# Optimization experiments

Measured on AMD Instinct MI355X. Metric: run time of the kernel, lower is better.

Reference implementation:

```python
import jax, jax.numpy as jnp
import numpy as np

H, W, C_IN, C_ADD = 721, 1440, 78, 8
N_NODES, K = 5882, 128
DAY_OF_YEAR = 182.5  # module default time_of_year
LN_EPS = 1e-5        # haiku LayerNorm default
NORM_EPS = 1e-7


def setup_inputs() -> dict:
    key = jax.random.key(0)
    ks = jax.random.split(key, 4)
    return {
        "var_grid": jax.random.normal(ks[0], (H, W, C_IN), dtype=jnp.float32),
        "nearby_idx": jax.random.randint(ks[1], (N_NODES, K), 0, H * W),
        "input_means": jnp.zeros((C_IN + C_ADD,), jnp.float32),
        "input_stds": jnp.ones((C_IN + C_ADD,), jnp.float32),
        "W1": jax.random.normal(ks[2], (C_IN + C_ADD, 256), dtype=jnp.float32) * 0.1,
        "b1": jnp.zeros((256,), jnp.float32),
        "ln_scale": jnp.ones((256,), jnp.float32),
        "ln_offset": jnp.zeros((256,), jnp.float32),
        "W2": jax.random.normal(ks[3], (256, 256), dtype=jnp.float32) * 0.1,
        "b2": jnp.zeros((256,), jnp.float32),
    }


def _additional_features(h, w):
    # 8 extra channels: sin/cos of lat/lon, normalized day-of-year, 3 zero pads
    lat = jnp.linspace(-90.0, 90.0, h)
    lon = jnp.linspace(0.0, 360.0, w)
    lat2d = jnp.broadcast_to(lat[:, None], (h, w))
    lon2d = jnp.broadcast_to(lon[None, :], (h, w))
    lat_r, lon_r = jnp.radians(lat2d), jnp.radians(lon2d)
    day = jnp.float32(DAY_OF_YEAR / 365.0)
    z = jnp.zeros((h, w), jnp.float32)
    return jnp.stack([
        jnp.sin(lat_r), jnp.cos(lat_r), jnp.sin(lon_r), jnp.cos(lon_r),
        jnp.full((h, w), day, jnp.float32), z, z, z,
    ], axis=-1)  # [H, W, 8]


def reference(var_grid, nearby_idx, input_means, input_stds,
              W1, b1, ln_scale, ln_offset, W2, b2):
    h, w, c = var_grid.shape
    add = _additional_features(h, w)                       # [H, W, 8]
    flat = jnp.concatenate([var_grid, add], -1).reshape(h * w, c + C_ADD)
    gathered = flat[nearby_idx]                            # [N, K, 86] irregular gather
    x = (gathered - input_means) / (input_stds + NORM_EPS)
    hidden = jax.nn.relu(jnp.einsum('nkc,cd->nkd', x, W1) + b1)
    mu = hidden.mean(-1, keepdims=True)
    var = hidden.var(-1, keepdims=True)
    hidden = (hidden - mu) * jax.lax.rsqrt(var + LN_EPS) * ln_scale + ln_offset
    nodes = jnp.einsum('nkd,de->nke', hidden, W2) + b2     # [N, K, 256]
    return nodes
```

## Files before the change

### kernel.cpp

```cpp
#include <hip/hip_runtime.h>
#include <hip/hip_bf16.h>
#include <math.h>

#define GH 721
#define GW 1440
#define C_IN 78
#define NNODES 5882
#define KNEIGH 128
#define M_TOTAL (NNODES * KNEIGH)
#define TM 128
#define NBLOCKS (M_TOTAL / TM)

typedef __attribute__((ext_vector_type(8))) short bf16x8;
typedef __attribute__((ext_vector_type(4))) float f32x4;

__device__ __forceinline__ unsigned short f2bf(float x) {
    __hip_bfloat16 b = __float2bfloat16(x);
    union { __hip_bfloat16 h; unsigned short u; } cv; cv.h = b; return cv.u;
}

__global__ void prep_kernel(const float* __restrict__ W1, const float* __restrict__ W2,
                            const float* __restrict__ means, const float* __restrict__ stds,
                            const float* __restrict__ b1,
                            unsigned short* __restrict__ bp1, unsigned short* __restrict__ bp2,
                            float* __restrict__ latT, float* __restrict__ lonT,
                            float* __restrict__ b1p)
{
    const int NB1 = 3 * 4 * 256 * 8;
    const int NB2 = 8 * 4 * 256 * 8;
    const int NTOT = NB1 + NB2 + GH + GW + 256;
    for (int e = blockIdx.x * blockDim.x + threadIdx.x; e < NTOT;
         e += gridDim.x * blockDim.x) {
        if (e < NB1) {
            int j = e & 7, c = (e >> 3) & 255, o = (e >> 11) & 3, s = e >> 13;
            int k = s * 32 + o * 8 + j;
            float v = 0.f;
            if (k < 82) v = W1[k * 256 + c] / (stds[k] + 1e-7f);
            bp1[e] = f2bf(v);
        } else if (e < NB1 + NB2) {
            int t = e - NB1;
            int j = t & 7, c = (t >> 3) & 255, o = (t >> 11) & 3, s = t >> 13;
            int k = s * 32 + o * 8 + j;
            bp2[t] = f2bf(W2[k * 256 + c]);
        } else if (e < NB1 + NB2 + GH) {
            int h = e - NB1 - NB2;
            float r = (-90.f + 0.25f * (float)h) * 0.017453292519943295f;
            latT[2 * h]     = sinf(r);
            latT[2 * h + 1] = cosf(r);
        } else if (e < NB1 + NB2 + GH + GW) {
            int w = e - NB1 - NB2 - GH;
            float r = ((float)w * (360.f / 1439.f)) * 0.017453292519943295f;
            lonT[2 * w]     = sinf(r);
            lonT[2 * w + 1] = cosf(r);
        } else {
            int c = e - NB1 - NB2 - GH - GW;
            float acc = b1[c];
            #pragma unroll 1
            for (int k = 0; k < 86; ++k) {
                float inv = 1.f / (stds[k] + 1e-7f);
                float w = W1[k * 256 + c] * inv;
                acc -= means[k] * w;
                if (k == 82) acc += 0.5f * w;
            }
            b1p[c] = acc;
        }
    }
}

__global__ __launch_bounds__(512, 4)
void fused_kernel(const float* __restrict__ var_grid, const int* __restrict__ idxs,
                  const unsigned short* __restrict__ bp1, const unsigned short* __restrict__ bp2,
                  const float* __restrict__ latT, const float* __restrict__ lonT,
                  const float* __restrict__ b1p, const float* __restrict__ lnS,
                  const float* __restrict__ lnO, const float* __restrict__ b2,
                  float* __restrict__ out)
{
    __shared__ __align__(16) char smem[TM * 256 * 2];
    __shared__ float red[2][4][TM];
    unsigned short* h_lds = (unsigned short*)smem;
    unsigned short (*x_lds)[104] = (unsigned short (*)[104])smem;
    float* otile = (float*)smem;

    const int tid  = threadIdx.x;
    const int lane = tid & 63;
    const int wave = tid >> 6;
    const int wr   = wave >> 2;
    const int wc   = wave & 3;
    const int l15  = lane & 15;
    const int lg   = lane >> 4;
    const int wbase = wc * 64;
    const int rbase = wr * 64;
    const long block0 = (long)blockIdx.x * TM;

    {
        const int row = tid >> 2, p = tid & 3;
        const int idx = idxs[block0 + row];
        const int hh = idx / GW;
        const int ww = idx - hh * GW;
        const float* src = var_grid + (long)idx * C_IN;
        float2 g[10];
        #pragma unroll
        for (int t = 0; t < 10; ++t) {
            const int q = p + 4 * t;
            if (q < 39) g[t] = *(const float2*)(src + 2 * q);
        }
        float2 tail;
        tail.x = latT[2 * hh]; tail.y = latT[2 * hh + 1];
        float2 tail2; tail2.x = lonT[2 * ww]; tail2.y = lonT[2 * ww + 1];
        unsigned int* xrow = (unsigned int*)&x_lds[row][0];
        #pragma unroll
        for (int t = 0; t < 12; ++t) {
            const int q = p + 4 * t;
            float v0, v1;
            if (q < 39)      { v0 = g[t].x; v1 = g[t].y; }
            else if (q == 39){ v0 = tail.x;  v1 = tail.y; }
            else if (q == 40){ v0 = tail2.x; v1 = tail2.y; }
            else             { v0 = 0.f; v1 = 0.f; }
            xrow[q] = ((unsigned int)f2bf(v1) << 16) | (unsigned int)f2bf(v0);
        }
    }

    float b1v[4], lsv[4], lov[4], b2v[4];
    #pragma unroll
    for (int nf = 0; nf < 4; ++nf) {
        int col = wbase + nf * 16 + l15;
        b1v[nf] = b1p[col]; lsv[nf] = lnS[col]; lov[nf] = lnO[col]; b2v[nf] = b2[col];
    }
    __syncthreads();

    f32x4 acc[4][4];
    #pragma unroll
    for (int mf = 0; mf < 4; ++mf)
        #pragma unroll
        for (int nf = 0; nf < 4; ++nf) acc[mf][nf] = (f32x4){0.f, 0.f, 0.f, 0.f};

    bf16x8 bw[4], bwn[4];
    #pragma unroll
    for (int nf = 0; nf < 4; ++nf)
        bw[nf] = *(const bf16x8*)(bp1 + ((size_t)(lg * 256) + wbase + nf * 16 + l15) * 8);

    #pragma unroll
    for (int s = 0; s < 3; ++s) {
        if (s < 2)
            #pragma unroll
            for (int nf = 0; nf < 4; ++nf)
                bwn[nf] = *(const bf16x8*)(bp1 + ((size_t)(((s + 1) * 4 + lg) * 256) + wbase + nf * 16 + l15) * 8);
        bf16x8 af[4];
        #pragma unroll
        for (int mf = 0; mf < 4; ++mf)
            af[mf] = *(const bf16x8*)&x_lds[rbase + mf * 16 + l15][s * 32 + lg * 8];
        #pragma unroll
        for (int mf = 0; mf < 4; ++mf)
            #pragma unroll
            for (int nf = 0; nf < 4; ++nf)
                acc[mf][nf] = __builtin_amdgcn_mfma_f32_16x16x32_bf16(af[mf], bw[nf], acc[mf][nf], 0, 0, 0);
        #pragma unroll
        for (int nf = 0; nf < 4; ++nf) bw[nf] = bwn[nf];
    }

    float sm[4][4], sq[4][4];
    #pragma unroll
    for (int mf = 0; mf < 4; ++mf)
        #pragma unroll
        for (int i = 0; i < 4; ++i) { sm[mf][i] = 0.f; sq[mf][i] = 0.f; }

    #pragma unroll
    for (int mf = 0; mf < 4; ++mf)
        #pragma unroll
        for (int nf = 0; nf < 4; ++nf)
            #pragma unroll
            for (int i = 0; i < 4; ++i) {
                float v = fmaxf(acc[mf][nf][i] + b1v[nf], 0.f);
                acc[mf][nf][i] = v;
                sm[mf][i] += v;
                sq[mf][i] += v * v;
            }

    #pragma unroll
    for (int m = 1; m < 16; m <<= 1)
        #pragma unroll
        for (int mf = 0; mf < 4; ++mf)
            #pragma unroll
            for (int i = 0; i < 4; ++i) {
                sm[mf][i] += __shfl_xor(sm[mf][i], m, 64);
                sq[mf][i] += __shfl_xor(sq[mf][i], m, 64);
            }

    if (l15 == 0) {
        #pragma unroll
        for (int mf = 0; mf < 4; ++mf)
            #pragma unroll
            for (int i = 0; i < 4; ++i) {
                int row = rbase + mf * 16 + lg * 4 + i;
                red[0][wc][row] = sm[mf][i];
                red[1][wc][row] = sq[mf][i];
            }
    }
    __syncthreads();

    #pragma unroll
    for (int mf = 0; mf < 4; ++mf)
        #pragma unroll
        for (int i = 0; i < 4; ++i) {
            int row = rbase + mf * 16 + lg * 4 + i;
            float tot = red[0][0][row] + red[0][1][row] + red[0][2][row] + red[0][3][row];
            float tq  = red[1][0][row] + red[1][1][row] + red[1][2][row] + red[1][3][row];
            float mean = tot * (1.f / 256.f);
            float var  = tq * (1.f / 256.f) - mean * mean;
            float rs = rsqrtf(var + 1e-5f);
            #pragma unroll
            for (int nf = 0; nf < 4; ++nf) {
                float v = (acc[mf][nf][i] - mean) * rs * lsv[nf] + lov[nf];
                int col = wbase + nf * 16 + l15;
                unsigned off = (unsigned)(row * 512 + col * 2);
                off ^= (unsigned)((row & 7) << 4);
                *(unsigned short*)((char*)h_lds + off) = f2bf(v);
            }
        }
    __syncthreads();

    #pragma unroll
    for (int mf = 0; mf < 4; ++mf)
        #pragma unroll
        for (int nf = 0; nf < 4; ++nf) acc[mf][nf] = (f32x4){0.f, 0.f, 0.f, 0.f};

    #pragma unroll
    for (int nf = 0; nf < 4; ++nf)
        bw[nf] = *(const bf16x8*)(bp2 + ((size_t)(lg * 256) + wbase + nf * 16 + l15) * 8);

    #pragma unroll
    for (int s = 0; s < 8; ++s) {
        if (s < 7)
            #pragma unroll
            for (int nf = 0; nf < 4; ++nf)
                bwn[nf] = *(const bf16x8*)(bp2 + ((size_t)(((s + 1) * 4 + lg) * 256) + wbase + nf * 16 + l15) * 8);
        bf16x8 af[4];
        #pragma unroll
        for (int mf = 0; mf < 4; ++mf) {
            int row = rbase + mf * 16 + l15;
            unsigned off = (unsigned)(row * 512 + (s * 32 + lg * 8) * 2);
            off ^= (unsigned)((row & 7) << 4);
            af[mf] = *(const bf16x8*)((char*)h_lds + off);
        }
        #pragma unroll
        for (int mf = 0; mf < 4; ++mf)
            #pragma unroll
            for (int nf = 0; nf < 4; ++nf)
                acc[mf][nf] = __builtin_amdgcn_mfma_f32_16x16x32_bf16(af[mf], bw[nf], acc[mf][nf], 0, 0, 0);
        #pragma unroll
        for (int nf = 0; nf < 4; ++nf) bw[nf] = bwn[nf];
    }

    #pragma unroll
    for (int p = 0; p < 4; ++p) {
        __syncthreads();
        if (wr == (p >> 1)) {
            #pragma unroll
            for (int mfl = 0; mfl < 2; ++mfl) {
                const int mf = (p & 1) * 2 + mfl;
                #pragma unroll
                for (int i = 0; i < 4; ++i) {
                    int rl = mfl * 16 + lg * 4 + i;
                    #pragma unroll
                    for (int nf = 0; nf < 4; ++nf) {
                        int col = wbase + nf * 16 + l15;
                        otile[rl * 256 + ((col + rl * 4) & 255)] = acc[mf][nf][i] + b2v[nf];
                    }
                }
            }
        }
        __syncthreads();
        #pragma unroll
        for (int r4 = 0; r4 < 4; ++r4) {
            const int rl = wave * 4 + r4;
            const long row_g = block0 + p * 32 + rl;
            f32x4 v = *(const f32x4*)&otile[rl * 256 + ((lane * 4 + rl * 4) & 255)];
            __builtin_nontemporal_store(v, (f32x4*)(out + row_g * 256 + lane * 4));
        }
    }
}

extern "C" void kernel_launch(void* const* d_in, const int* in_sizes, int n_in,
                              void* d_out, int out_size, void* d_ws, size_t ws_size,
                              hipStream_t stream) {
    const float* var_grid = (const float*)d_in[0];
    const int*   idxs     = (const int*)d_in[1];
    const float* means    = (const float*)d_in[2];
    const float* stds     = (const float*)d_in[3];
    const float* W1       = (const float*)d_in[4];
    const float* b1       = (const float*)d_in[5];
    const float* lnS      = (const float*)d_in[6];
    const float* lnO      = (const float*)d_in[7];
    const float* W2       = (const float*)d_in[8];
    const float* b2       = (const float*)d_in[9];
    float* out = (float*)d_out;

    char* ws = (char*)d_ws;
    unsigned short* bp1 = (unsigned short*)ws;
    unsigned short* bp2 = (unsigned short*)(ws + 49152);
    float* latT = (float*)(ws + 180224);
    float* lonT = (float*)(ws + 186000);
    float* b1p  = (float*)(ws + 197520);

    prep_kernel<<<362, 256, 0, stream>>>(W1, W2, means, stds, b1, bp1, bp2, latT, lonT, b1p);
    fused_kernel<<<NBLOCKS, 512, 0, stream>>>(var_grid, idxs, bp1, bp2, latT, lonT,
                                              b1p, lnS, lnO, b2, out);
}
```

Baseline: 524.1 us.

## Remap blocks per XCD and store MFMA results directly to global memory

Block indices are remapped so that each of the 8 XCDs handles a contiguous range of row tiles (5882 blocks split as 736/735). The epilogue no longer stages the output through LDS with barriers and vectorized nontemporal stores. Each lane now writes its accumulator values straight to global memory as scalar stores of 16 consecutive floats per row segment. This removes the LDS round trip and 8 barriers, but gives up 16-byte coalesced nontemporal writes for narrower scattered stores on a write-bound output.

```diff
diff --git a/kernel.cpp b/kernel.cpp
--- a/kernel.cpp
+++ b/kernel.cpp
@@ -79,7 +79,11 @@
     __shared__ float red[2][4][TM];
     unsigned short* h_lds = (unsigned short*)smem;
     unsigned short (*x_lds)[104] = (unsigned short (*)[104])smem;
-    float* otile = (float*)smem;
+
+    const int q_ = 735, r_ = 2;
+    const int xcd = blockIdx.x & 7;
+    const int ii  = blockIdx.x >> 3;
+    const int swz = (xcd < r_ ? xcd * (q_ + 1) : r_ * (q_ + 1) + (xcd - r_) * q_) + ii;
 
     const int tid  = threadIdx.x;
     const int lane = tid & 63;
@@ -90,7 +94,7 @@
     const int lg   = lane >> 4;
     const int wbase = wc * 64;
     const int rbase = wr * 64;
-    const long block0 = (long)blockIdx.x * TM;
+    const long block0 = (long)swz * TM;
 
     {
         const int row = tid >> 2, p = tid & 3;
@@ -98,23 +102,22 @@
         const int hh = idx / GW;
         const int ww = idx - hh * GW;
         const float* src = var_grid + (long)idx * C_IN;
-        float2 g[10];
+        float2 g[10], tl, tl2;
         #pragma unroll
         for (int t = 0; t < 10; ++t) {
             const int q = p + 4 * t;
             if (q < 39) g[t] = *(const float2*)(src + 2 * q);
         }
-        float2 tail;
-        tail.x = latT[2 * hh]; tail.y = latT[2 * hh + 1];
-        float2 tail2; tail2.x = lonT[2 * ww]; tail2.y = lonT[2 * ww + 1];
+        tl.x  = latT[2 * hh]; tl.y  = latT[2 * hh + 1];
+        tl2.x = lonT[2 * ww]; tl2.y = lonT[2 * ww + 1];
         unsigned int* xrow = (unsigned int*)&x_lds[row][0];
         #pragma unroll
         for (int t = 0; t < 12; ++t) {
             const int q = p + 4 * t;
             float v0, v1;
             if (q < 39)      { v0 = g[t].x; v1 = g[t].y; }
-            else if (q == 39){ v0 = tail.x;  v1 = tail.y; }
-            else if (q == 40){ v0 = tail2.x; v1 = tail2.y; }
+            else if (q == 39){ v0 = tl.x;  v1 = tl.y; }
+            else if (q == 40){ v0 = tl2.x; v1 = tl2.y; }
             else             { v0 = 0.f; v1 = 0.f; }
             xrow[q] = ((unsigned int)f2bf(v1) << 16) | (unsigned int)f2bf(v0);
         }
@@ -252,32 +255,15 @@
     }
 
     #pragma unroll
-    for (int p = 0; p < 4; ++p) {
-        __syncthreads();
-        if (wr == (p >> 1)) {
-            #pragma unroll
-            for (int mfl = 0; mfl < 2; ++mfl) {
-                const int mf = (p & 1) * 2 + mfl;
-                #pragma unroll
-                for (int i = 0; i < 4; ++i) {
-                    int rl = mfl * 16 + lg * 4 + i;
-                    #pragma unroll
-                    for (int nf = 0; nf < 4; ++nf) {
-                        int col = wbase + nf * 16 + l15;
-                        otile[rl * 256 + ((col + rl * 4) & 255)] = acc[mf][nf][i] + b2v[nf];
-                    }
-                }
-            }
-        }
-        __syncthreads();
-        #pragma unroll
-        for (int r4 = 0; r4 < 4; ++r4) {
-            const int rl = wave * 4 + r4;
-            const long row_g = block0 + p * 32 + rl;
-            f32x4 v = *(const f32x4*)&otile[rl * 256 + ((lane * 4 + rl * 4) & 255)];
-            __builtin_nontemporal_store(v, (f32x4*)(out + row_g * 256 + lane * 4));
-        }
-    }
+    for (int mf = 0; mf < 4; ++mf)
+        #pragma unroll
+        for (int i = 0; i < 4; ++i) {
+            long row_g = block0 + rbase + mf * 16 + lg * 4 + i;
+            float* po = out + row_g * 256 + wbase;
+            #pragma unroll
+            for (int nf = 0; nf < 4; ++nf)
+                po[nf * 16 + l15] = acc[mf][nf][i] + b2v[nf];
+        }
 }
 
 extern "C" void kernel_launch(void* const* d_in, const int* in_sizes, int n_in,
```

After: 459.7 us. -12.3%, faster.
